# Kernel optimization log

Measured on AMD Instinct MI355X. Metric: run time of the kernel, lower is better.

## Reference

```python
import jax, jax.numpy as jnp
import numpy as np

N = 32768          # nodes
E = 131072         # edges
H = 4              # heads
RNA = 128          # rna_feature_dim
PROT = 32          # prot_feature_dim
F0 = 64            # num_features_per_layer[0] == [1]
CIN = F0 + PROT    # cross-path feature dim (96)
LRELU = 0.2


def _param(key, shape):
    return jax.random.normal(key, shape, dtype=jnp.float32) * 0.1


def setup_inputs() -> dict:
    key = jax.random.key(0)
    ks = jax.random.split(key, 20)
    return {
        "rna_data": jax.random.normal(ks[0], (N, RNA), dtype=jnp.float32),
        "prot_data": jax.random.normal(ks[1], (N, PROT), dtype=jnp.float32),
        "edge_index": jax.random.randint(ks[2], (2, E), 0, N, dtype=jnp.int32),
        "W_gat_proj": _param(ks[3], (RNA, F0)),
        "b_gat_proj": _param(ks[4], (F0,)),
        "W_gat_reproj": _param(ks[5], (F0, RNA)),
        "b_gat_reproj": _param(ks[6], (RNA,)),
        "Wg": _param(ks[7], (F0, H * F0)),
        "ag_src": _param(ks[8], (H, F0)),
        "ag_trg": _param(ks[9], (H, F0)),
        "bg": _param(ks[10], (F0,)),
        "W_cross_proj": _param(ks[11], (RNA + PROT, CIN)),
        "b_cross_proj": _param(ks[12], (CIN,)),
        "W_cross_reproj": _param(ks[13], (CIN, RNA + PROT)),
        "b_cross_reproj": _param(ks[14], (RNA + PROT,)),
        "Wc": _param(ks[15], (CIN, H * CIN)),
        "ac_src": _param(ks[16], (H, CIN)),
        "ac_trg": _param(ks[17], (H, CIN)),
        "bc": _param(ks[18], (CIN,)),
    }


def gat_layer(x, W, a_src, a_trg, bias, edge_index, softmax_on_src):
    """GATLayer with concat=False, activation=None, skip connection (in==out dim),
    dropout in eval mode. CrossAttnLayer groups the edge-softmax by src instead of trg."""
    n, f = x.shape
    src, trg = edge_index[0], edge_index[1]
    proj = (x @ W).reshape(n, H, f)                               # [N,H,F] lift targets
    s_src = jnp.einsum('nhf,hf->nh', proj, a_src)                 # [N,H]
    s_trg = jnp.einsum('nhf,hf->nh', proj, a_trg)                 # [N,H]
    scores = jax.nn.leaky_relu(s_src[src] + s_trg[trg], LRELU)    # [E,H] per-edge scores
    grp = src if softmax_on_src else trg
    ex = jnp.exp(scores - scores.max())                           # global-max shift (as in source)
    denom = jax.ops.segment_sum(ex, grp, num_segments=n)          # [N,H]
    attn = ex / (denom[grp] + 1e-16)                              # neighborhood-aware softmax [E,H]
    weighted = proj[src] * attn[:, :, None]                       # [E,H,F]
    out = jax.ops.segment_sum(weighted, trg, num_segments=n)      # scatter-add aggregate [N,H,F]
    out = out + x[:, None, :]                                     # direct skip (out_dim == in_dim)
    out = out.mean(axis=1) + bias                                 # concat=False -> head mean, + bias
    return out                                                    # activation=None (last layer)


def reference(rna_data, prot_data, edge_index,
              W_gat_proj, b_gat_proj, W_gat_reproj, b_gat_reproj,
              Wg, ag_src, ag_trg, bg,
              W_cross_proj, b_cross_proj, W_cross_reproj, b_cross_reproj,
              Wc, ac_src, ac_trg, bc):
    concat = jnp.concatenate([rna_data, prot_data], axis=1)       # [N, RNA+PROT]
    rna_p = rna_data @ W_gat_proj + b_gat_proj                    # [N, F0]
    cross_p = concat @ W_cross_proj + b_cross_proj                # [N, CIN]
    gat_out = gat_layer(rna_p, Wg, ag_src, ag_trg, bg, edge_index, False)    # [N, F0]
    cross_out = gat_layer(cross_p, Wc, ac_src, ac_trg, bc, edge_index, True)  # [N, CIN]
    # CrossAttnLayer's trailing view(-1, num_heads, num_out_features)
    cross_out = cross_out.reshape(-1, H, CIN)                     # [N/H, H, CIN]
    gat_final = gat_out @ W_gat_reproj + b_gat_reproj             # [N, RNA]
    cross_final = cross_out @ W_cross_reproj + b_cross_reproj     # [N/H, H, RNA+PROT]
    return gat_final, cross_final
```

## Files before the change

### kernel.cpp

```cpp
#include <hip/hip_runtime.h>
#include <hip/hip_bf16.h>

#define NN 32768
#define NE 131072
#define HH 4

constexpr float kLrelu = 0.2f;

using bf16x8 = __attribute__((ext_vector_type(8))) __bf16;
using f32x4  = __attribute__((ext_vector_type(4))) float;

__device__ inline short f2b(float f) {
    __hip_bfloat16 h = __float2bfloat16(f);
    return __builtin_bit_cast(short, h);
}
__device__ inline float b2f(short s) {
    __hip_bfloat16 h = __builtin_bit_cast(__hip_bfloat16, s);
    return __bfloat162float(h);
}
__device__ inline float blo(int u) {
    return __builtin_bit_cast(float, (int)(u << 16));
}
__device__ inline float bhi(int u) {
    return __builtin_bit_cast(float, (int)(u & 0xffff0000));
}
__device__ inline float lrexp(float x) {
    return __expf(x > 0.f ? x : kLrelu * x);
}

template<int K, int LDA, int OUTN, int BM, int BN, bool BF16OUT>
__global__ __launch_bounds__(256) void mfma_gemm(
    const short* __restrict__ A, const short* __restrict__ Wt,
    const float* __restrict__ bias,
    float* __restrict__ Cf, short* __restrict__ Cb)
{
    constexpr int KP    = K + 8;
    constexpr int WM    = BM / 32;
    constexpr int WN    = 4 / WM;
    constexpr int WBN   = BN / WN;
    constexpr int CF    = WBN / 16;
    constexpr int CPR   = K / 8;
    constexpr int TOT   = (BM + BN) * KP;
    constexpr int SLICE = TOT / 4;

    __shared__ short lds[TOT];
    short* As = lds;
    short* Bs = lds + BM * KP;

    const int tid  = threadIdx.x;
    const int wave = tid >> 6;
    const int lane = tid & 63;
    const int lr   = lane & 15;
    const int kb   = lane >> 4;
    const int wm   = wave % WM;
    const int wn   = wave / WM;
    const int row0 = blockIdx.x * BM;
    const int col0 = blockIdx.y * BN;

    #pragma unroll
    for (int g = tid; g < BM * CPR; g += 256) {
        int r = g / CPR, c = g - r * CPR;
        bf16x8 v = *(const bf16x8*)(A + (size_t)(row0 + r) * LDA + c * 8);
        *(bf16x8*)(As + r * KP + c * 8) = v;
    }
    #pragma unroll
    for (int g = tid; g < BN * CPR; g += 256) {
        int r = g / CPR, c = g - r * CPR;
        bf16x8 v = *(const bf16x8*)(Wt + (size_t)(col0 + r) * K + c * 8);
        *(bf16x8*)(Bs + r * KP + c * 8) = v;
    }
    __syncthreads();

    f32x4 acc[2][CF] = {};
    #pragma unroll
    for (int k0 = 0; k0 < K; k0 += 32) {
        bf16x8 af0 = *(const bf16x8*)(As + (wm * 32 + lr     ) * KP + k0 + kb * 8);
        bf16x8 af1 = *(const bf16x8*)(As + (wm * 32 + lr + 16) * KP + k0 + kb * 8);
        #pragma unroll
        for (int cf = 0; cf < CF; ++cf) {
            bf16x8 bv = *(const bf16x8*)(Bs + (wn * WBN + cf * 16 + lr) * KP + k0 + kb * 8);
            acc[0][cf] = __builtin_amdgcn_mfma_f32_16x16x32_bf16(af0, bv, acc[0][cf], 0, 0, 0);
            acc[1][cf] = __builtin_amdgcn_mfma_f32_16x16x32_bf16(af1, bv, acc[1][cf], 0, 0, 0);
        }
    }

    #pragma unroll
    for (int mf = 0; mf < 2; ++mf) {
        __syncthreads();
        if constexpr (BF16OUT) {
            constexpr int LEP = WBN + 8;
            short* ep = lds + wave * SLICE;
            #pragma unroll
            for (int cf = 0; cf < CF; ++cf) {
                const int c  = cf * 16 + lr;
                const float bv = bias ? bias[col0 + wn * WBN + c] : 0.0f;
                #pragma unroll
                for (int j = 0; j < 4; ++j)
                    ep[(kb * 4 + j) * LEP + c] = f2b(acc[mf][cf][j] + bv);
            }
            __syncthreads();
            constexpr int CROW = WBN / 8;
            for (int g = lane; g < 16 * CROW; g += 64) {
                int r = g / CROW, cc = g - r * CROW;
                bf16x8 v = *(const bf16x8*)(ep + r * LEP + cc * 8);
                *(bf16x8*)(Cb + (size_t)(row0 + wm * 32 + mf * 16 + r) * OUTN
                              + col0 + wn * WBN + cc * 8) = v;
            }
        } else {
            constexpr int LEPF = WBN + 4;
            float* epf = (float*)(lds + wave * SLICE);
            #pragma unroll
            for (int cf = 0; cf < CF; ++cf) {
                const int c  = cf * 16 + lr;
                const float bv = bias ? bias[col0 + wn * WBN + c] : 0.0f;
                #pragma unroll
                for (int j = 0; j < 4; ++j)
                    epf[(kb * 4 + j) * LEPF + c] = acc[mf][cf][j] + bv;
            }
            __syncthreads();
            constexpr int CROWF = WBN / 4;
            for (int g = lane; g < 16 * CROWF; g += 64) {
                int r = g / CROWF, cc = g - r * CROWF;
                float4 v = *(const float4*)(epf + r * LEPF + cc * 4);
                *(float4*)(Cf + (size_t)(row0 + wm * 32 + mf * 16 + r) * OUTN
                              + col0 + wn * WBN + cc * 4) = v;
            }
        }
    }
}

template<int F>
__global__ __launch_bounds__(256) void scores_proj(
    const short* __restrict__ proj_b,
    const float* __restrict__ a_src, const float* __restrict__ a_trg,
    float* __restrict__ ssrc, float* __restrict__ strg)
{
    int t = blockIdx.x * 256 + threadIdx.x;
    if (t >= NN * HH) return;
    int n = t >> 2, h = t & 3;
    const int4* p = (const int4*)(proj_b + (size_t)n * (4 * F) + h * F);
    const float* as = a_src + h * F;
    const float* at = a_trg + h * F;
    float ss = 0.f, st = 0.f;
    #pragma unroll
    for (int c = 0; c < F / 8; ++c) {
        int4 v = p[c];
        int u[4] = { v.x, v.y, v.z, v.w };
        #pragma unroll
        for (int q = 0; q < 4; ++q) {
            float x0 = blo(u[q]), x1 = bhi(u[q]);
            ss += x0 * as[c * 8 + 2 * q] + x1 * as[c * 8 + 2 * q + 1];
            st += x0 * at[c * 8 + 2 * q] + x1 * at[c * 8 + 2 * q + 1];
        }
    }
    ssrc[t] = ss;
    strg[t] = st;
}

__global__ __launch_bounds__(256) void wt_all_kernel(
    const float* W0, const float* W1, const float* W2,
    const float* W3, const float* W4, const float* W5,
    short* T0, short* T1, short* T2, short* T3, short* T4, short* T5)
{
    int K, N; const float* W; short* T;
    switch (blockIdx.y) {
        case 0: K = 128; N =  64; W = W0; T = T0; break;
        case 1: K =  64; N = 256; W = W1; T = T1; break;
        case 2: K =  64; N = 128; W = W2; T = T2; break;
        case 3: K = 160; N =  96; W = W3; T = T3; break;
        case 4: K =  96; N = 384; W = W4; T = T4; break;
        default:K =  96; N = 160; W = W5; T = T5; break;
    }
    int t = blockIdx.x * 256 + threadIdx.x;
    if (t >= K * N) return;
    int n = t / K, k = t - n * K;
    T[t] = f2b(W[(size_t)k * N + n]);
}

__global__ __launch_bounds__(256) void concat_kernel(
    const float* __restrict__ rna, const float* __restrict__ prot,
    short* __restrict__ cb)
{
    int t = blockIdx.x * 256 + threadIdx.x;
    if (t >= NN * 40) return;
    int n = t / 40, j = (t - n * 40) * 4;
    float4 v = (j < 128) ? *(const float4*)(rna  + (size_t)n * 128 + j)
                         : *(const float4*)(prot + (size_t)n * 32 + (j - 128));
    short4 o = { f2b(v.x), f2b(v.y), f2b(v.z), f2b(v.w) };
    *(short4*)(cb + (size_t)n * 160 + j) = o;
}

__global__ __launch_bounds__(256) void zero_kernel(int4* __restrict__ p)
{
    p[blockIdx.x * 256 + threadIdx.x] = make_int4(0, 0, 0, 0);
}

__global__ __launch_bounds__(256) void hist_dual(const int* __restrict__ ei,
                                                 int* __restrict__ deg_t,
                                                 int* __restrict__ deg_s)
{
    int e = blockIdx.x * 256 + threadIdx.x;
    if (e >= NE) return;
    atomicAdd(&deg_s[ei[e]], 1);
    atomicAdd(&deg_t[ei[NE + e]], 1);
}

__global__ __launch_bounds__(1024) void scan_dual(
    const int* __restrict__ deg_t, int* __restrict__ rowptr_t, int* __restrict__ cursor_t,
    const int* __restrict__ deg_s, int* __restrict__ rowptr_s, int* __restrict__ cursor_s)
{
    const int* deg    = blockIdx.x ? deg_s    : deg_t;
    int*       rowptr = blockIdx.x ? rowptr_s : rowptr_t;
    int*       cursor = blockIdx.x ? cursor_s : cursor_t;
    __shared__ int sums[1024];
    const int t = threadIdx.x;
    const int base = t * 32;
    int local[32];
    int s = 0;
    #pragma unroll
    for (int i = 0; i < 32; ++i) { local[i] = s; s += deg[base + i]; }
    sums[t] = s;
    __syncthreads();
    for (int off = 1; off < 1024; off <<= 1) {
        int v = (t >= off) ? sums[t - off] : 0;
        __syncthreads();
        sums[t] += v;
        __syncthreads();
    }
    const int prev = (t == 0) ? 0 : sums[t - 1];
    #pragma unroll
    for (int i = 0; i < 32; ++i) {
        rowptr[base + i] = prev + local[i];
        cursor[base + i] = prev + local[i];
    }
    if (t == 1023) rowptr[NN] = prev + s;
}

__global__ __launch_bounds__(256) void scatter_dual(
    const int* __restrict__ ei,
    int* __restrict__ cursor_t, int* __restrict__ csr_srcT,
    int* __restrict__ cursor_s, int* __restrict__ csr_trgS,
    int* __restrict__ map_s2t)
{
    int e = blockIdx.x * 256 + threadIdx.x;
    if (e >= NE) return;
    int s = ei[e], t = ei[NE + e];
    int st = atomicAdd(&cursor_t[t], 1);
    csr_srcT[st] = s;
    int ss = atomicAdd(&cursor_s[s], 1);
    csr_trgS[ss] = t;
    map_s2t[ss]  = st;
}

__global__ __launch_bounds__(256) void gat_denattn(
    const int* __restrict__ rowptr_t, const int* __restrict__ csr_srcT,
    const float* __restrict__ ssrc, const float* __restrict__ strg,
    float* __restrict__ attnT)
{
    int n = blockIdx.x * 256 + threadIdx.x;
    if (n >= NN) return;
    const int beg = rowptr_t[n], end = rowptr_t[n + 1];
    const float4 stv = *(const float4*)(strg + 4 * (size_t)n);
    float d0 = 0.f, d1 = 0.f, d2 = 0.f, d3 = 0.f;
    for (int sl = beg; sl < end; ++sl) {
        const int s = csr_srcT[sl];
        const float4 sv = *(const float4*)(ssrc + 4 * (size_t)s);
        d0 += lrexp(sv.x + stv.x); d1 += lrexp(sv.y + stv.y);
        d2 += lrexp(sv.z + stv.z); d3 += lrexp(sv.w + stv.w);
    }
    const float r0 = 1.f / (d0 + 1e-16f), r1 = 1.f / (d1 + 1e-16f);
    const float r2 = 1.f / (d2 + 1e-16f), r3 = 1.f / (d3 + 1e-16f);
    for (int sl = beg; sl < end; ++sl) {
        const int s = csr_srcT[sl];
        const float4 sv = *(const float4*)(ssrc + 4 * (size_t)s);
        *(float4*)(attnT + 4 * (size_t)sl) =
            make_float4(lrexp(sv.x + stv.x) * r0, lrexp(sv.y + stv.y) * r1,
                        lrexp(sv.z + stv.z) * r2, lrexp(sv.w + stv.w) * r3);
    }
}

__global__ __launch_bounds__(256) void cross_denattn(
    const int* __restrict__ rowptr_s, const int* __restrict__ csr_trgS,
    const int* __restrict__ map_s2t,
    const float* __restrict__ ssrc, const float* __restrict__ strg,
    float* __restrict__ attnT)
{
    int n = blockIdx.x * 256 + threadIdx.x;
    if (n >= NN) return;
    const int beg = rowptr_s[n], end = rowptr_s[n + 1];
    const float4 ssv = *(const float4*)(ssrc + 4 * (size_t)n);
    float d0 = 0.f, d1 = 0.f, d2 = 0.f, d3 = 0.f;
    for (int sl = beg; sl < end; ++sl) {
        const int t = csr_trgS[sl];
        const float4 tv = *(const float4*)(strg + 4 * (size_t)t);
        d0 += lrexp(ssv.x + tv.x); d1 += lrexp(ssv.y + tv.y);
        d2 += lrexp(ssv.z + tv.z); d3 += lrexp(ssv.w + tv.w);
    }
    const float r0 = 1.f / (d0 + 1e-16f), r1 = 1.f / (d1 + 1e-16f);
    const float r2 = 1.f / (d2 + 1e-16f), r3 = 1.f / (d3 + 1e-16f);
    for (int sl = beg; sl < end; ++sl) {
        const int t = csr_trgS[sl];
        const float4 tv = *(const float4*)(strg + 4 * (size_t)t);
        *(float4*)(attnT + 4 * (size_t)map_s2t[sl]) =
            make_float4(lrexp(ssv.x + tv.x) * r0, lrexp(ssv.y + tv.y) * r1,
                        lrexp(ssv.z + tv.z) * r2, lrexp(ssv.w + tv.w) * r3);
    }
}

template<int F, int NPB>
__global__ __launch_bounds__(F * NPB) void aggregate_lean(
    const int* __restrict__ rowptr_t, const int* __restrict__ csr_srcT,
    const float* __restrict__ attnT, const short* __restrict__ proj_b,
    const short* __restrict__ x_pb, const float* __restrict__ bias,
    short* __restrict__ aggb)
{
    const int f    = threadIdx.x;
    const int node = blockIdx.x * NPB + threadIdx.y;
    const int beg  = rowptr_t[node], end = rowptr_t[node + 1];
    float acc = 0.f;

    int sl = beg;
    for (; sl + 2 <= end; sl += 2) {
        const float4 a0 = *(const float4*)(attnT + 4 * (size_t)sl);
        const float4 a1 = *(const float4*)(attnT + 4 * (size_t)(sl + 1));
        const int s0 = csr_srcT[sl];
        const int s1 = csr_srcT[sl + 1];
        const short* p0 = proj_b + (size_t)s0 * (4 * F) + f;
        const short* p1 = proj_b + (size_t)s1 * (4 * F) + f;
        acc += a0.x * b2f(p0[0]) + a0.y * b2f(p0[F])
             + a0.z * b2f(p0[2 * F]) + a0.w * b2f(p0[3 * F]);
        acc += a1.x * b2f(p1[0]) + a1.y * b2f(p1[F])
             + a1.z * b2f(p1[2 * F]) + a1.w * b2f(p1[3 * F]);
    }
    if (sl < end) {
        const float4 a0 = *(const float4*)(attnT + 4 * (size_t)sl);
        const int s0 = csr_srcT[sl];
        const short* p0 = proj_b + (size_t)s0 * (4 * F) + f;
        acc += a0.x * b2f(p0[0]) + a0.y * b2f(p0[F])
             + a0.z * b2f(p0[2 * F]) + a0.w * b2f(p0[3 * F]);
    }
    const int o = node * F + f;
    aggb[o] = f2b(acc * 0.25f + b2f(x_pb[o]) + bias[f]);
}

extern "C" void kernel_launch(void* const* d_in, const int* in_sizes, int n_in,
                              void* d_out, int out_size, void* d_ws, size_t ws_size,
                              hipStream_t stream)
{
    const float* rna   = (const float*)d_in[0];
    const float* prot  = (const float*)d_in[1];
    const int*   ei    = (const int*)  d_in[2];
    const float* Wgp   = (const float*)d_in[3];
    const float* bgp   = (const float*)d_in[4];
    const float* Wgr   = (const float*)d_in[5];
    const float* bgr   = (const float*)d_in[6];
    const float* Wg    = (const float*)d_in[7];
    const float* ags   = (const float*)d_in[8];
    const float* agt   = (const float*)d_in[9];
    const float* bg    = (const float*)d_in[10];
    const float* Wcp   = (const float*)d_in[11];
    const float* bcp   = (const float*)d_in[12];
    const float* Wcr   = (const float*)d_in[13];
    const float* bcr   = (const float*)d_in[14];
    const float* Wc    = (const float*)d_in[15];
    const float* acs   = (const float*)d_in[16];
    const float* act   = (const float*)d_in[17];
    const float* bc    = (const float*)d_in[18];

    float* out_gat   = (float*)d_out;
    float* out_cross = out_gat + (size_t)NN * 128;

    float* attnT  = (float*)d_ws;
    float* ssrc   = attnT + (size_t)NE * 4;
    float* strg   = ssrc + (size_t)NN * 4;
    short* proj_b = (short*)(strg + (size_t)NN * 4);
    short* cb     = proj_b + (size_t)NN * 384;
    short* x_pb   = cb    + (size_t)NN * 160;
    short* aggb   = x_pb  + (size_t)NN * 96;
    short* wt_gp  = aggb  + (size_t)NN * 96;
    short* wt_g   = wt_gp + 128 * 64;
    short* wt_gr  = wt_g  + 64 * 256;
    short* wt_cp  = wt_gr + 64 * 128;
    short* wt_c   = wt_cp + 160 * 96;
    short* wt_cr  = wt_c  + 96 * 384;
    int*   deg_t  = (int*)(wt_cr + 96 * 160);
    int*   deg_s  = deg_t  + NN;
    int*   cursor_t = deg_s  + NN;
    int*   cursor_s = cursor_t + NN;
    int*   rowptr_t = cursor_s + NN;
    int*   rowptr_s = rowptr_t + NN + 1;
    int*   csr_srcT = rowptr_s + NN + 1;
    int*   csr_trgS = csr_srcT + NE;
    int*   map_s2t  = csr_trgS + NE;

    concat_kernel<<<(NN * 40 + 255) / 256, 256, 0, stream>>>(rna, prot, cb);
    wt_all_kernel<<<dim3(144, 6), 256, 0, stream>>>(Wgp, Wg, Wgr, Wcp, Wc, Wcr,
                                                    wt_gp, wt_g, wt_gr, wt_cp, wt_c, wt_cr);
    zero_kernel<<<(2 * NN) / (256 * 4), 256, 0, stream>>>((int4*)deg_t);
    hist_dual<<<NE / 256, 256, 0, stream>>>(ei, deg_t, deg_s);
    scan_dual<<<2, 1024, 0, stream>>>(deg_t, rowptr_t, cursor_t, deg_s, rowptr_s, cursor_s);
    scatter_dual<<<NE / 256, 256, 0, stream>>>(ei, cursor_t, csr_srcT,
                                               cursor_s, csr_trgS, map_s2t);

    mfma_gemm<128, 160,  64, 128,  64, true ><<<dim3(256, 1), 256, 0, stream>>>(cb,   wt_gp, bgp, nullptr, x_pb);
    mfma_gemm< 64,  64, 256, 128, 128, true ><<<dim3(256, 2), 256, 0, stream>>>(x_pb, wt_g,  nullptr, nullptr, proj_b);
    scores_proj<64><<<(NN * HH) / 256, 256, 0, stream>>>(proj_b, ags, agt, ssrc, strg);
    gat_denattn<<<NN / 256, 256, 0, stream>>>(rowptr_t, csr_srcT, ssrc, strg, attnT);
    aggregate_lean<64, 4><<<NN / 4, dim3(64, 4), 0, stream>>>(
        rowptr_t, csr_srcT, attnT, proj_b, x_pb, bg, aggb);
    mfma_gemm< 64,  64, 128, 128, 128, false><<<dim3(256, 1), 256, 0, stream>>>(aggb, wt_gr, bgr, out_gat, nullptr);

    mfma_gemm<160, 160,  96,  64,  96, true ><<<dim3(512, 1), 256, 0, stream>>>(cb,   wt_cp, bcp, nullptr, x_pb);
    mfma_gemm< 96,  96, 384, 128, 128, true ><<<dim3(256, 3), 256, 0, stream>>>(x_pb, wt_c,  nullptr, nullptr, proj_b);
    scores_proj<96><<<(NN * HH) / 256, 256, 0, stream>>>(proj_b, acs, act, ssrc, strg);
    cross_denattn<<<NN / 256, 256, 0, stream>>>(rowptr_s, csr_trgS, map_s2t, ssrc, strg, attnT);
    aggregate_lean<96, 2><<<NN / 2, dim3(96, 2), 0, stream>>>(
        rowptr_t, csr_srcT, attnT, proj_b, x_pb, bc, aggb);
    mfma_gemm< 96,  96, 160, 128,  80, false><<<dim3(256, 2), 256, 0, stream>>>(aggb, wt_cr, bcr, out_cross, nullptr);
}
```

Baseline: 206.6 us.

## Fuse softmax into aggregation, merge prep kernels, retile GEMMs

Removes the per-edge attention buffer and the map_s2t indirection. The GAT path now computes the edge exponentials and the per-target denominator inside the aggregation kernel, while the cross path first stores only per-source reciprocal denominators and recomputes the exponentials during aggregation. Aggregation threads now handle two features each with packed bf16 loads and stores, and the concat, weight-transpose and zeroing kernels are merged into one launch. The GEMM tile M sizes and grids are also changed. Exponentials are recomputed for every edge, which adds ALU work in exchange for less memory traffic and fewer launches.

```diff
diff --git a/kernel.cpp b/kernel.cpp
--- a/kernel.cpp
+++ b/kernel.cpp
@@ -157,42 +157,41 @@
     strg[t] = st;
 }
 
-__global__ __launch_bounds__(256) void wt_all_kernel(
+__global__ __launch_bounds__(256) void prep_kernel(
+    const float* __restrict__ rna, const float* __restrict__ prot,
+    short* __restrict__ cb,
     const float* W0, const float* W1, const float* W2,
     const float* W3, const float* W4, const float* W5,
-    short* T0, short* T1, short* T2, short* T3, short* T4, short* T5)
-{
-    int K, N; const float* W; short* T;
-    switch (blockIdx.y) {
-        case 0: K = 128; N =  64; W = W0; T = T0; break;
-        case 1: K =  64; N = 256; W = W1; T = T1; break;
-        case 2: K =  64; N = 128; W = W2; T = T2; break;
-        case 3: K = 160; N =  96; W = W3; T = T3; break;
-        case 4: K =  96; N = 384; W = W4; T = T4; break;
-        default:K =  96; N = 160; W = W5; T = T5; break;
-    }
-    int t = blockIdx.x * 256 + threadIdx.x;
-    if (t >= K * N) return;
-    int n = t / K, k = t - n * K;
-    T[t] = f2b(W[(size_t)k * N + n]);
-}
-
-__global__ __launch_bounds__(256) void concat_kernel(
-    const float* __restrict__ rna, const float* __restrict__ prot,
-    short* __restrict__ cb)
-{
-    int t = blockIdx.x * 256 + threadIdx.x;
-    if (t >= NN * 40) return;
-    int n = t / 40, j = (t - n * 40) * 4;
-    float4 v = (j < 128) ? *(const float4*)(rna  + (size_t)n * 128 + j)
-                         : *(const float4*)(prot + (size_t)n * 32 + (j - 128));
-    short4 o = { f2b(v.x), f2b(v.y), f2b(v.z), f2b(v.w) };
-    *(short4*)(cb + (size_t)n * 160 + j) = o;
-}
-
-__global__ __launch_bounds__(256) void zero_kernel(int4* __restrict__ p)
-{
-    p[blockIdx.x * 256 + threadIdx.x] = make_int4(0, 0, 0, 0);
+    short* T0, short* T1, short* T2, short* T3, short* T4, short* T5,
+    int4* __restrict__ zero_p)
+{
+    const int bid = blockIdx.x;
+    if (bid < 5120) {
+        int t = bid * 256 + threadIdx.x;
+        int n = t / 40, j = (t - n * 40) * 4;
+        float4 v = (j < 128) ? *(const float4*)(rna  + (size_t)n * 128 + j)
+                             : *(const float4*)(prot + (size_t)n * 32 + (j - 128));
+        short4 o = { f2b(v.x), f2b(v.y), f2b(v.z), f2b(v.w) };
+        *(short4*)(cb + (size_t)n * 160 + j) = o;
+    } else if (bid < 5984) {
+        int idx = bid - 5120;
+        int wsel = idx / 144, sub = idx - wsel * 144;
+        int K, N; const float* W; short* T;
+        switch (wsel) {
+            case 0: K = 128; N =  64; W = W0; T = T0; break;
+            case 1: K =  64; N = 256; W = W1; T = T1; break;
+            case 2: K =  64; N = 128; W = W2; T = T2; break;
+            case 3: K = 160; N =  96; W = W3; T = T3; break;
+            case 4: K =  96; N = 384; W = W4; T = T4; break;
+            default:K =  96; N = 160; W = W5; T = T5; break;
+        }
+        int t = sub * 256 + threadIdx.x;
+        if (t >= K * N) return;
+        int n = t / K, k = t - n * K;
+        T[t] = f2b(W[(size_t)k * N + n]);
+    } else {
+        zero_p[(bid - 5984) * 256 + threadIdx.x] = make_int4(0, 0, 0, 0);
+    }
 }
 
 __global__ __launch_bounds__(256) void hist_dual(const int* __restrict__ ei,
@@ -239,8 +238,7 @@
 __global__ __launch_bounds__(256) void scatter_dual(
     const int* __restrict__ ei,
     int* __restrict__ cursor_t, int* __restrict__ csr_srcT,
-    int* __restrict__ cursor_s, int* __restrict__ csr_trgS,
-    int* __restrict__ map_s2t)
+    int* __restrict__ cursor_s, int* __restrict__ csr_trgS)
 {
     int e = blockIdx.x * 256 + threadIdx.x;
     if (e >= NE) return;
@@ -249,98 +247,86 @@
     csr_srcT[st] = s;
     int ss = atomicAdd(&cursor_s[s], 1);
     csr_trgS[ss] = t;
-    map_s2t[ss]  = st;
-}
-
-__global__ __launch_bounds__(256) void gat_denattn(
-    const int* __restrict__ rowptr_t, const int* __restrict__ csr_srcT,
+}
+
+__global__ __launch_bounds__(256) void den_src_kernel(
+    const int* __restrict__ rowptr_s, const int* __restrict__ csr_trgS,
     const float* __restrict__ ssrc, const float* __restrict__ strg,
-    float* __restrict__ attnT)
-{
-    int n = blockIdx.x * 256 + threadIdx.x;
-    if (n >= NN) return;
-    const int beg = rowptr_t[n], end = rowptr_t[n + 1];
-    const float4 stv = *(const float4*)(strg + 4 * (size_t)n);
-    float d0 = 0.f, d1 = 0.f, d2 = 0.f, d3 = 0.f;
-    for (int sl = beg; sl < end; ++sl) {
-        const int s = csr_srcT[sl];
-        const float4 sv = *(const float4*)(ssrc + 4 * (size_t)s);
-        d0 += lrexp(sv.x + stv.x); d1 += lrexp(sv.y + stv.y);
-        d2 += lrexp(sv.z + stv.z); d3 += lrexp(sv.w + stv.w);
-    }
-    const float r0 = 1.f / (d0 + 1e-16f), r1 = 1.f / (d1 + 1e-16f);
-    const float r2 = 1.f / (d2 + 1e-16f), r3 = 1.f / (d3 + 1e-16f);
-    for (int sl = beg; sl < end; ++sl) {
-        const int s = csr_srcT[sl];
-        const float4 sv = *(const float4*)(ssrc + 4 * (size_t)s);
-        *(float4*)(attnT + 4 * (size_t)sl) =
-            make_float4(lrexp(sv.x + stv.x) * r0, lrexp(sv.y + stv.y) * r1,
-                        lrexp(sv.z + stv.z) * r2, lrexp(sv.w + stv.w) * r3);
-    }
-}
-
-__global__ __launch_bounds__(256) void cross_denattn(
-    const int* __restrict__ rowptr_s, const int* __restrict__ csr_trgS,
-    const int* __restrict__ map_s2t,
-    const float* __restrict__ ssrc, const float* __restrict__ strg,
-    float* __restrict__ attnT)
+    float* __restrict__ recip)
 {
     int n = blockIdx.x * 256 + threadIdx.x;
     if (n >= NN) return;
     const int beg = rowptr_s[n], end = rowptr_s[n + 1];
-    const float4 ssv = *(const float4*)(ssrc + 4 * (size_t)n);
+    const float4 sv = *(const float4*)(ssrc + 4 * (size_t)n);
     float d0 = 0.f, d1 = 0.f, d2 = 0.f, d3 = 0.f;
     for (int sl = beg; sl < end; ++sl) {
         const int t = csr_trgS[sl];
         const float4 tv = *(const float4*)(strg + 4 * (size_t)t);
-        d0 += lrexp(ssv.x + tv.x); d1 += lrexp(ssv.y + tv.y);
-        d2 += lrexp(ssv.z + tv.z); d3 += lrexp(ssv.w + tv.w);
-    }
-    const float r0 = 1.f / (d0 + 1e-16f), r1 = 1.f / (d1 + 1e-16f);
-    const float r2 = 1.f / (d2 + 1e-16f), r3 = 1.f / (d3 + 1e-16f);
-    for (int sl = beg; sl < end; ++sl) {
-        const int t = csr_trgS[sl];
-        const float4 tv = *(const float4*)(strg + 4 * (size_t)t);
-        *(float4*)(attnT + 4 * (size_t)map_s2t[sl]) =
-            make_float4(lrexp(ssv.x + tv.x) * r0, lrexp(ssv.y + tv.y) * r1,
-                        lrexp(ssv.z + tv.z) * r2, lrexp(ssv.w + tv.w) * r3);
-    }
-}
-
-template<int F, int NPB>
-__global__ __launch_bounds__(F * NPB) void aggregate_lean(
+        d0 += lrexp(sv.x + tv.x); d1 += lrexp(sv.y + tv.y);
+        d2 += lrexp(sv.z + tv.z); d3 += lrexp(sv.w + tv.w);
+    }
+    *(float4*)(recip + 4 * (size_t)n) =
+        make_float4(1.f / (d0 + 1e-16f), 1.f / (d1 + 1e-16f),
+                    1.f / (d2 + 1e-16f), 1.f / (d3 + 1e-16f));
+}
+
+template<int F, int NPB, bool GROUP_SRC>
+__global__ __launch_bounds__((F / 2) * NPB) void aggregate_fused(
     const int* __restrict__ rowptr_t, const int* __restrict__ csr_srcT,
-    const float* __restrict__ attnT, const short* __restrict__ proj_b,
+    const float* __restrict__ ssrc, const float* __restrict__ strg,
+    const float* __restrict__ recip,
+    const short* __restrict__ proj_b,
     const short* __restrict__ x_pb, const float* __restrict__ bias,
     short* __restrict__ aggb)
 {
-    const int f    = threadIdx.x;
+    const int f2   = threadIdx.x * 2;
     const int node = blockIdx.x * NPB + threadIdx.y;
     const int beg  = rowptr_t[node], end = rowptr_t[node + 1];
-    float acc = 0.f;
-
-    int sl = beg;
-    for (; sl + 2 <= end; sl += 2) {
-        const float4 a0 = *(const float4*)(attnT + 4 * (size_t)sl);
-        const float4 a1 = *(const float4*)(attnT + 4 * (size_t)(sl + 1));
-        const int s0 = csr_srcT[sl];
-        const int s1 = csr_srcT[sl + 1];
-        const short* p0 = proj_b + (size_t)s0 * (4 * F) + f;
-        const short* p1 = proj_b + (size_t)s1 * (4 * F) + f;
-        acc += a0.x * b2f(p0[0]) + a0.y * b2f(p0[F])
-             + a0.z * b2f(p0[2 * F]) + a0.w * b2f(p0[3 * F]);
-        acc += a1.x * b2f(p1[0]) + a1.y * b2f(p1[F])
-             + a1.z * b2f(p1[2 * F]) + a1.w * b2f(p1[3 * F]);
-    }
-    if (sl < end) {
-        const float4 a0 = *(const float4*)(attnT + 4 * (size_t)sl);
-        const int s0 = csr_srcT[sl];
-        const short* p0 = proj_b + (size_t)s0 * (4 * F) + f;
-        acc += a0.x * b2f(p0[0]) + a0.y * b2f(p0[F])
-             + a0.z * b2f(p0[2 * F]) + a0.w * b2f(p0[3 * F]);
-    }
-    const int o = node * F + f;
-    aggb[o] = f2b(acc * 0.25f + b2f(x_pb[o]) + bias[f]);
+    const float4 stv = *(const float4*)(strg + 4 * (size_t)node);
+
+    float a0 = 0.f, a1 = 0.f;
+    float h0l = 0.f, h1l = 0.f, h2l = 0.f, h3l = 0.f;
+    float h0h = 0.f, h1h = 0.f, h2h = 0.f, h3h = 0.f;
+    float d0 = 0.f, d1 = 0.f, d2 = 0.f, d3 = 0.f;
+
+    #pragma unroll 2
+    for (int sl = beg; sl < end; ++sl) {
+        const int s = csr_srcT[sl];
+        const float4 sv = *(const float4*)(ssrc + 4 * (size_t)s);
+        float e0 = lrexp(sv.x + stv.x);
+        float e1 = lrexp(sv.y + stv.y);
+        float e2 = lrexp(sv.z + stv.z);
+        float e3 = lrexp(sv.w + stv.w);
+        const short* p = proj_b + (size_t)s * (4 * F) + f2;
+        const int u0 = *(const int*)(p);
+        const int u1 = *(const int*)(p + F);
+        const int u2 = *(const int*)(p + 2 * F);
+        const int u3 = *(const int*)(p + 3 * F);
+        if constexpr (GROUP_SRC) {
+            const float4 rc = *(const float4*)(recip + 4 * (size_t)s);
+            e0 *= rc.x; e1 *= rc.y; e2 *= rc.z; e3 *= rc.w;
+            a0 += e0 * blo(u0) + e1 * blo(u1) + e2 * blo(u2) + e3 * blo(u3);
+            a1 += e0 * bhi(u0) + e1 * bhi(u1) + e2 * bhi(u2) + e3 * bhi(u3);
+        } else {
+            d0 += e0; d1 += e1; d2 += e2; d3 += e3;
+            h0l += e0 * blo(u0); h0h += e0 * bhi(u0);
+            h1l += e1 * blo(u1); h1h += e1 * bhi(u1);
+            h2l += e2 * blo(u2); h2h += e2 * bhi(u2);
+            h3l += e3 * blo(u3); h3h += e3 * bhi(u3);
+        }
+    }
+    if constexpr (!GROUP_SRC) {
+        const float r0 = 1.f / (d0 + 1e-16f), r1 = 1.f / (d1 + 1e-16f);
+        const float r2 = 1.f / (d2 + 1e-16f), r3 = 1.f / (d3 + 1e-16f);
+        a0 = h0l * r0 + h1l * r1 + h2l * r2 + h3l * r3;
+        a1 = h0h * r0 + h1h * r1 + h2h * r2 + h3h * r3;
+    }
+    const int o = node * F + f2;
+    const int ux = *(const int*)(x_pb + o);
+    const float v0 = a0 * 0.25f + blo(ux) + bias[f2];
+    const float v1 = a1 * 0.25f + bhi(ux) + bias[f2 + 1];
+    const int packed = (f2b(v0) & 0xffff) | ((int)f2b(v1) << 16);
+    *(int*)(aggb + o) = packed;
 }
 
 extern "C" void kernel_launch(void* const* d_in, const int* in_sizes, int n_in,
@@ -370,10 +356,10 @@
     float* out_gat   = (float*)d_out;
     float* out_cross = out_gat + (size_t)NN * 128;
 
-    float* attnT  = (float*)d_ws;
-    float* ssrc   = attnT + (size_t)NE * 4;
+    float* ssrc   = (float*)d_ws;
     float* strg   = ssrc + (size_t)NN * 4;
-    short* proj_b = (short*)(strg + (size_t)NN * 4);
+    float* recip  = strg + (size_t)NN * 4;
+    short* proj_b = (short*)(recip + (size_t)NN * 4);
     short* cb     = proj_b + (size_t)NN * 384;
     short* x_pb   = cb    + (size_t)NN * 160;
     short* aggb   = x_pb  + (size_t)NN * 96;
@@ -391,30 +377,27 @@
     int*   rowptr_s = rowptr_t + NN + 1;
     int*   csr_srcT = rowptr_s + NN + 1;
     int*   csr_trgS = csr_srcT + NE;
-    int*   map_s2t  = csr_trgS + NE;
-
-    concat_kernel<<<(NN * 40 + 255) / 256, 256, 0, stream>>>(rna, prot, cb);
-    wt_all_kernel<<<dim3(144, 6), 256, 0, stream>>>(Wgp, Wg, Wgr, Wcp, Wc, Wcr,
-                                                    wt_gp, wt_g, wt_gr, wt_cp, wt_c, wt_cr);
-    zero_kernel<<<(2 * NN) / (256 * 4), 256, 0, stream>>>((int4*)deg_t);
+
+    prep_kernel<<<6048, 256, 0, stream>>>(rna, prot, cb,
+                                          Wgp, Wg, Wgr, Wcp, Wc, Wcr,
+                                          wt_gp, wt_g, wt_gr, wt_cp, wt_c, wt_cr,
+                                          (int4*)deg_t);
     hist_dual<<<NE / 256, 256, 0, stream>>>(ei, deg_t, deg_s);
     scan_dual<<<2, 1024, 0, stream>>>(deg_t, rowptr_t, cursor_t, deg_s, rowptr_s, cursor_s);
-    scatter_dual<<<NE / 256, 256, 0, stream>>>(ei, cursor_t, csr_srcT,
-                                               cursor_s, csr_trgS, map_s2t);
-
-    mfma_gemm<128, 160,  64, 128,  64, true ><<<dim3(256, 1), 256, 0, stream>>>(cb,   wt_gp, bgp, nullptr, x_pb);
-    mfma_gemm< 64,  64, 256, 128, 128, true ><<<dim3(256, 2), 256, 0, stream>>>(x_pb, wt_g,  nullptr, nullptr, proj_b);
+    scatter_dual<<<NE / 256, 256, 0, stream>>>(ei, cursor_t, csr_srcT, cursor_s, csr_trgS);
+
+    mfma_gemm<128, 160,  64, 32,  64, true ><<<dim3(1024, 1), 256, 0, stream>>>(cb,   wt_gp, bgp, nullptr, x_pb);
+    mfma_gemm< 64,  64, 256, 64, 128, true ><<<dim3( 512, 2), 256, 0, stream>>>(x_pb, wt_g,  nullptr, nullptr, proj_b);
     scores_proj<64><<<(NN * HH) / 256, 256, 0, stream>>>(proj_b, ags, agt, ssrc, strg);
-    gat_denattn<<<NN / 256, 256, 0, stream>>>(rowptr_t, csr_srcT, ssrc, strg, attnT);
-    aggregate_lean<64, 4><<<NN / 4, dim3(64, 4), 0, stream>>>(
-        rowptr_t, csr_srcT, attnT, proj_b, x_pb, bg, aggb);
-    mfma_gemm< 64,  64, 128, 128, 128, false><<<dim3(256, 1), 256, 0, stream>>>(aggb, wt_gr, bgr, out_gat, nullptr);
-
-    mfma_gemm<160, 160,  96,  64,  96, true ><<<dim3(512, 1), 256, 0, stream>>>(cb,   wt_cp, bcp, nullptr, x_pb);
-    mfma_gemm< 96,  96, 384, 128, 128, true ><<<dim3(256, 3), 256, 0, stream>>>(x_pb, wt_c,  nullptr, nullptr, proj_b);
+    aggregate_fused<64, 8, false><<<NN / 8, dim3(32, 8), 0, stream>>>(
+        rowptr_t, csr_srcT, ssrc, strg, nullptr, proj_b, x_pb, bg, aggb);
+    mfma_gemm< 64,  64, 128, 64,  64, false><<<dim3( 512, 2), 256, 0, stream>>>(aggb, wt_gr, bgr, out_gat, nullptr);
+
+    mfma_gemm<160, 160,  96, 64,  96, true ><<<dim3( 512, 1), 256, 0, stream>>>(cb,   wt_cp, bcp, nullptr, x_pb);
+    mfma_gemm< 96,  96, 384, 64, 128, true ><<<dim3( 512, 3), 256, 0, stream>>>(x_pb, wt_c,  nullptr, nullptr, proj_b);
     scores_proj<96><<<(NN * HH) / 256, 256, 0, stream>>>(proj_b, acs, act, ssrc, strg);
-    cross_denattn<<<NN / 256, 256, 0, stream>>>(rowptr_s, csr_trgS, map_s2t, ssrc, strg, attnT);
-    aggregate_lean<96, 2><<<NN / 2, dim3(96, 2), 0, stream>>>(
-        rowptr_t, csr_srcT, attnT, proj_b, x_pb, bc, aggb);
-    mfma_gemm< 96,  96, 160, 128,  80, false><<<dim3(256, 2), 256, 0, stream>>>(aggb, wt_cr, bcr, out_cross, nullptr);
-}
+    den_src_kernel<<<NN / 256, 256, 0, stream>>>(rowptr_s, csr_trgS, ssrc, strg, recip);
+    aggregate_fused<96, 8, true><<<NN / 8, dim3(48, 8), 0, stream>>>(
+        rowptr_t, csr_srcT, ssrc, strg, recip, proj_b, x_pb, bc, aggb);
+    mfma_gemm< 96,  96, 160, 64, 160, false><<<dim3( 512, 1), 256, 0, stream>>>(aggb, wt_cr, bcr, out_cross, nullptr);
+}
```

Result: faster. 178.1 us (-13.8%).
